# Optimization experiments

Measured on AMD Instinct MI355X. Metric: run time of the kernel, lower is better.

The kernel has to match this reference:

```python
import jax, jax.numpy as jnp
import numpy as np

B, S, C = 4, 4096, 1024   # batch, input_size (seq len), channels
H, D, DK = 16, 64, 256    # nhead, head dim, dim_k (Linformer projection)


def setup_inputs() -> dict:
    key = jax.random.key(0)
    ks = jax.random.split(key, 9)
    s_in = 1.0 / np.sqrt(C)
    s_e = 1.0 / np.sqrt(S)
    return {
        'x':   jax.random.normal(ks[0], (B, S, C), jnp.float32),
        # per-head Q/K/V projection weights (Linear(channels, dim, bias=False))
        'Wq':  jax.random.normal(ks[1], (H, D, C), jnp.float32) * s_in,
        'Wk':  jax.random.normal(ks[2], (H, D, C), jnp.float32) * s_in,
        'Wv':  jax.random.normal(ks[3], (H, D, C), jnp.float32) * s_in,
        # shared (layerwise) E/F Linear(input_size, dim_k) with bias
        'E_w': jax.random.normal(ks[4], (DK, S), jnp.float32) * s_e,
        'E_b': jnp.zeros((DK,), jnp.float32),
        'F_w': jax.random.normal(ks[5], (DK, S), jnp.float32) * s_e,
        'F_b': jnp.zeros((DK,), jnp.float32),
        # output projection Linear(dim*nhead, channels)
        'Wo':  jax.random.normal(ks[6], (C, H * D), jnp.float32) * (1.0 / np.sqrt(H * D)),
        'bo':  jnp.zeros((C,), jnp.float32),
    }


def reference(x, Wq, Wk, Wv, E_w, E_b, F_w, F_b, Wo, bo):
    b, s, c = x.shape
    h, d, _ = Wq.shape
    # per-head projections (vectorized over the Python head loop)
    Q = jnp.einsum('bsc,hdc->bhsd', x, Wq)            # [B,H,S,D]
    Kt = jnp.einsum('bsc,hdc->bhds', x, Wk)           # K already transposed: [B,H,D,S]
    Vt = jnp.einsum('bsc,hdc->bhds', x, Wv)           # [B,H,D,S]
    # Linformer low-rank projections along the sequence axis
    Kp = jnp.einsum('bhds,ks->bhdk', Kt, E_w) + E_b   # [B,H,D,DK]
    Vp = jnp.einsum('bhds,ks->bhdk', Vt, F_w) + F_b   # [B,H,D,DK]
    scores = jnp.einsum('bhsd,bhdk->bhsk', Q, Kp) / jnp.sqrt(jnp.asarray(d, x.dtype))
    P = jax.nn.softmax(scores, axis=-1)               # softmax over projected dim_k
    head_out = jnp.einsum('bhsk,bhdk->bhsd', P, Vp)   # [B,H,S,D]
    out = head_out.transpose(0, 2, 1, 3).reshape(b, s, h * d)  # concat heads
    return out @ Wo.T + bo
```

## Files before the change

### kernel.cpp

```cpp
#include <hip/hip_runtime.h>
#include <stdint.h>

typedef __attribute__((ext_vector_type(8))) short bf16x8;
typedef __attribute__((ext_vector_type(4))) float f32x4;
typedef __attribute__((ext_vector_type(16))) float f32x16;

__device__ __forceinline__ unsigned short f2b(float f) {
  union { float f; uint32_t u; } v; v.f = f;
  uint32_t u = v.u;
  return (unsigned short)((u + 0x7FFFu + ((u >> 16) & 1u)) >> 16);
}

__device__ __forceinline__ void gll16(const unsigned short* gsrc, unsigned short* lds_uniform) {
  __builtin_amdgcn_global_load_lds(
      (const __attribute__((address_space(1))) uint32_t*)gsrc,
      (__attribute__((address_space(3))) uint32_t*)lds_uniform,
      16, 0, 0);
}

#define MFMA(a, b, c) __builtin_amdgcn_mfma_f32_16x16x32_bf16((a), (b), (c), 0, 0, 0)
#define MFMA32(a, b, c) __builtin_amdgcn_mfma_f32_32x32x16_bf16((a), (b), (c), 0, 0, 0)

__global__ void cast_x_dual(const float* __restrict__ x,
                            unsigned short* __restrict__ xb,
                            unsigned short* __restrict__ xT) {
  __shared__ unsigned short tile[64][65];
  const int st = blockIdx.x * 64;
  const int ct = blockIdx.y * 64;
  const int b = blockIdx.z;
  const int t = threadIdx.x;
#pragma unroll
  for (int it = 0; it < 4; ++it) {
    int linear = (it * 256 + t) * 4;
    int r = linear >> 6, c = linear & 63;
    float4 v = *(const float4*)(x + ((size_t)(b * 4096 + st + r)) * 1024 + ct + c);
    ushort4 o;
    o.x = f2b(v.x); o.y = f2b(v.y); o.z = f2b(v.z); o.w = f2b(v.w);
    *(ushort4*)(xb + ((size_t)(b * 4096 + st + r)) * 1024 + ct + c) = o;
    tile[r][c] = o.x; tile[r][c + 1] = o.y; tile[r][c + 2] = o.z; tile[r][c + 3] = o.w;
  }
  __syncthreads();
#pragma unroll
  for (int it = 0; it < 4; ++it) {
    int linear = (it * 256 + t) * 4;
    int r = linear >> 6, c = linear & 63;
    ushort4 o;
    o.x = tile[c][r]; o.y = tile[c + 1][r]; o.z = tile[c + 2][r]; o.w = tile[c + 3][r];
    *(ushort4*)(xT + ((size_t)b * 1024 + ct + r) * 4096 + st + c) = o;
  }
}

__global__ void cast6(const float* __restrict__ s0, const float* __restrict__ s1,
                      const float* __restrict__ s2, const float* __restrict__ s3,
                      const float* __restrict__ s4, const float* __restrict__ s5,
                      const float* __restrict__ E_b, const float* __restrict__ F_b,
                      unsigned short* __restrict__ d0, unsigned short* __restrict__ d1,
                      unsigned short* __restrict__ d2, unsigned short* __restrict__ d3,
                      unsigned short* __restrict__ d4, unsigned short* __restrict__ d5,
                      float* __restrict__ EFbias) {
  if (blockIdx.y == 6) {
    if (blockIdx.x == 0) {
      int t = threadIdx.x;
      EFbias[t] = E_b[t];
      EFbias[256 + t] = F_b[t];
    }
    return;
  }
  const float* src; unsigned short* dst; float sc = 1.0f;
  switch (blockIdx.y) {
    case 0: src = s0; dst = d0; sc = 0.18033688011112042f; break;
    case 1: src = s1; dst = d1; break;
    case 2: src = s2; dst = d2; break;
    case 3: src = s3; dst = d3; break;
    case 4: src = s4; dst = d4; break;
    default: src = s5; dst = d5; break;
  }
  int i = (blockIdx.x * 256 + threadIdx.x) * 4;
  float4 v = *(const float4*)(src + i);
  ushort4 o;
  o.x = f2b(v.x * sc); o.y = f2b(v.y * sc); o.z = f2b(v.z * sc); o.w = f2b(v.w * sc);
  *(ushort4*)(dst + i) = o;
}

template <int BIAS, bool OBF16>
__global__ __launch_bounds__(512, 1) void gemm_bt256(
    const unsigned short* __restrict__ A, const unsigned short* __restrict__ B,
    void* __restrict__ Cout, const float* __restrict__ bias,
    int K, int lda, int ldb, int ldc) {
  __shared__ unsigned short Asm_[4][256 * 32];
  __shared__ unsigned short Bsm_[4][256 * 32];
  const int tid = threadIdx.x;
  const int wave = tid >> 6, lane = tid & 63;
  const int g = (lane >> 4) & 3, l15 = lane & 15;
  const int wmi = wave >> 2, wni = wave & 3;
  const int bm = blockIdx.x * 256, bn = blockIdx.y * 256;

  const int c0 = wave * 2;
  const int rr0 = c0 * 16 + (lane >> 2);
  const int rr1 = rr0 + 16;
  const int sl0 = (lane & 3) ^ ((rr0 >> 1) & 3);
  const int sl1 = (lane & 3) ^ ((rr1 >> 1) & 3);

#define STG(T, BUF)                                                                   \
  {                                                                                   \
    int kt_ = (T) * 32;                                                               \
    gll16(A + (size_t)(bm + rr0) * lda + kt_ + sl0 * 8, Asm_[BUF] + c0 * 512);        \
    gll16(B + (size_t)(bn + rr0) * ldb + kt_ + sl0 * 8, Bsm_[BUF] + c0 * 512);        \
    gll16(A + (size_t)(bm + rr1) * lda + kt_ + sl1 * 8, Asm_[BUF] + (c0 + 1) * 512);  \
    gll16(B + (size_t)(bn + rr1) * ldb + kt_ + sl1 * 8, Bsm_[BUF] + (c0 + 1) * 512);  \
  }

  f32x4 acc[8][4];
#pragma unroll
  for (int i = 0; i < 8; ++i)
#pragma unroll
    for (int j = 0; j < 4; ++j) acc[i][j] = (f32x4){0.f, 0.f, 0.f, 0.f};

  const int nt = K >> 5;
  STG(0, 0);
  if (nt > 1) STG(1, 1);
  if (nt > 2) STG(2, 2);
  asm volatile("s_waitcnt vmcnt(8)" ::: "memory");
  __builtin_amdgcn_s_barrier();
  asm volatile("" ::: "memory");

  for (int t = 0; t < nt; ++t) {
    const int cur = t & 3;
    const char* Ac = (const char*)Asm_[cur];
    const char* Bc = (const char*)Bsm_[cur];

    bf16x8 afr[8], bfr[4];
#pragma unroll
    for (int mf = 0; mf < 8; ++mf) {
      int m = wmi * 128 + mf * 16 + l15;
      afr[mf] = *(const bf16x8*)(Ac + m * 64 + ((g ^ ((m >> 1) & 3)) << 4));
    }
#pragma unroll
    for (int nf = 0; nf < 4; ++nf) {
      int n = wni * 64 + nf * 16 + l15;
      bfr[nf] = *(const bf16x8*)(Bc + n * 64 + ((g ^ ((n >> 1) & 3)) << 4));
    }

    if (t + 3 < nt) STG(t + 3, (t + 3) & 3);

    __builtin_amdgcn_s_setprio(1);
#pragma unroll
    for (int mf = 0; mf < 8; ++mf)
#pragma unroll
      for (int nf = 0; nf < 4; ++nf)
        acc[mf][nf] = MFMA(afr[mf], bfr[nf], acc[mf][nf]);
    __builtin_amdgcn_s_setprio(0);

    if (t + 3 < nt)      asm volatile("s_waitcnt vmcnt(8)" ::: "memory");
    else if (t + 2 < nt) asm volatile("s_waitcnt vmcnt(4)" ::: "memory");
    else                 asm volatile("s_waitcnt vmcnt(0)" ::: "memory");
    __builtin_amdgcn_s_barrier();
    asm volatile("" ::: "memory");
  }
#undef STG

#pragma unroll
  for (int mf = 0; mf < 8; ++mf)
#pragma unroll
    for (int r = 0; r < 4; ++r) {
      int row = bm + wmi * 128 + mf * 16 + g * 4 + r;
      float rb = (BIAS == 1) ? bias[row] : 0.f;
#pragma unroll
      for (int nf = 0; nf < 4; ++nf) {
        int col = bn + wni * 64 + nf * 16 + l15;
        float v = acc[mf][nf][r] + rb + ((BIAS == 2) ? bias[col] : 0.f);
        if (OBF16) ((unsigned short*)Cout)[(size_t)row * ldc + col] = f2b(v);
        else       ((float*)Cout)[(size_t)row * ldc + col] = v;
      }
    }
}

__global__ __launch_bounds__(256, 2) void gemm_xef_splitk(
    const unsigned short* __restrict__ A,
    const unsigned short* __restrict__ B,
    float* __restrict__ Cpart) {
  __shared__ unsigned short Asm_[2][128 * 32];
  __shared__ unsigned short Bsm_[2][128 * 32];
  const int tid = threadIdx.x;
  const int wave = tid >> 6, lane = tid & 63;
  const int g = lane >> 4, l15 = lane & 15;
  const int bm = blockIdx.x * 128, bn = blockIdx.y * 128;
  const int z = blockIdx.z, split = z >> 2, b = z & 3;
  const unsigned short* Ab = A + split * 1024;
  const unsigned short* Bb = B + (size_t)b * 1024 * 4096 + split * 1024;
  const int wm = (wave >> 1) * 64, wn = (wave & 1) * 64;

  const int rr0 = wave * 16 + (lane >> 2);
  const int rr1 = rr0 + 64;
  const int sl0 = (lane & 3) ^ ((rr0 >> 1) & 3);
  const int sl1 = (lane & 3) ^ ((rr1 >> 1) & 3);

#define XEF_STAGE(T, BUF)                                                           \
  {                                                                                 \
    int kt_ = (T) * 32;                                                             \
    gll16(Ab + (size_t)(bm + rr0) * 4096 + kt_ + sl0 * 8, Asm_[BUF] + wave * 512);  \
    gll16(Bb + (size_t)(bn + rr0) * 4096 + kt_ + sl0 * 8, Bsm_[BUF] + wave * 512);  \
    gll16(Ab + (size_t)(bm + rr1) * 4096 + kt_ + sl1 * 8, Asm_[BUF] + (wave + 4) * 512); \
    gll16(Bb + (size_t)(bn + rr1) * 4096 + kt_ + sl1 * 8, Bsm_[BUF] + (wave + 4) * 512); \
  }

  f32x4 acc[4][4];
#pragma unroll
  for (int i = 0; i < 4; ++i)
#pragma unroll
    for (int j = 0; j < 4; ++j) acc[i][j] = (f32x4){0.f, 0.f, 0.f, 0.f};

  const int nt = 32;
  XEF_STAGE(0, 0);
  for (int t = 0; t < nt; ++t) {
    const int cur = t & 1;
    if (t + 1 < nt) {
      XEF_STAGE(t + 1, cur ^ 1);
      asm volatile("s_waitcnt vmcnt(4)" ::: "memory");
    } else {
      asm volatile("s_waitcnt vmcnt(0)" ::: "memory");
    }
    __builtin_amdgcn_s_barrier();
    asm volatile("" ::: "memory");

    bf16x8 af[4], bfr[4];
    const char* Ac = (const char*)Asm_[cur];
    const char* Bc = (const char*)Bsm_[cur];
#pragma unroll
    for (int mi = 0; mi < 4; ++mi) {
      int m = wm + mi * 16 + l15;
      af[mi] = *(const bf16x8*)(Ac + m * 64 + ((g ^ ((m >> 1) & 3)) << 4));
    }
#pragma unroll
    for (int ni = 0; ni < 4; ++ni) {
      int n = wn + ni * 16 + l15;
      bfr[ni] = *(const bf16x8*)(Bc + n * 64 + ((g ^ ((n >> 1) & 3)) << 4));
    }
#pragma unroll
    for (int mi = 0; mi < 4; ++mi)
#pragma unroll
      for (int ni = 0; ni < 4; ++ni)
        acc[mi][ni] = MFMA(af[mi], bfr[ni], acc[mi][ni]);

    asm volatile("" ::: "memory");
    __builtin_amdgcn_s_barrier();
  }
#undef XEF_STAGE

  float* C = Cpart + (size_t)z * (512 * 1024);
#pragma unroll
  for (int mi = 0; mi < 4; ++mi)
#pragma unroll
    for (int r = 0; r < 4; ++r) {
      int row = bm + wm + mi * 16 + g * 4 + r;
#pragma unroll
      for (int ni = 0; ni < 4; ++ni) {
        int col = bn + wn + ni * 16 + l15;
        C[(size_t)row * 1024 + col] = acc[mi][ni][r];
      }
    }
}

__global__ void reduce_xef(const float* __restrict__ P,
                           const float* __restrict__ bias,
                           unsigned short* __restrict__ out) {
  int t = blockIdx.x * 256 + threadIdx.x;
  size_t flat = (size_t)t * 4;
  float4 s = *(const float4*)(P + flat);
#pragma unroll
  for (int sp = 1; sp < 4; ++sp) {
    float4 v = *(const float4*)(P + (size_t)sp * 2097152 + flat);
    s.x += v.x; s.y += v.y; s.z += v.z; s.w += v.w;
  }
  float rb = bias[(flat >> 10) & 511];
  ushort4 o;
  o.x = f2b(s.x + rb); o.y = f2b(s.y + rb);
  o.z = f2b(s.z + rb); o.w = f2b(s.w + rb);
  *(ushort4*)(out + flat) = o;
}

template <int BIAS, bool OBF16, int CMODE>
__global__ __launch_bounds__(256, 4) void gemm_bt64(
    const unsigned short* __restrict__ A, const unsigned short* __restrict__ B,
    void* __restrict__ Cout, const float* __restrict__ bias,
    int M, int N, int K, int lda, int ldb, int ldc,
    long long sA, long long sB, long long sC) {
  __shared__ unsigned short Asm_[2][64 * 32];
  __shared__ unsigned short Bsm_[2][64 * 32];
  const int tid = threadIdx.x;
  const int wave = tid >> 6, lane = tid & 63;
  const int g = lane >> 4, l15 = lane & 15;
  const int bm = blockIdx.x * 64, bn = blockIdx.y * 64;
  const unsigned short* Ab = A + (size_t)blockIdx.z * sA;
  const unsigned short* Bb = B + (size_t)blockIdx.z * sB;
  const int wm = (wave >> 1) * 32, wn = (wave & 1) * 32;

  const int rr = wave * 16 + (lane >> 2);
  const int sl = (lane & 3) ^ ((rr >> 1) & 3);

#define BT64_STAGE(T, BUF)                                                      \
  {                                                                             \
    int kt_ = (T) * 32;                                                         \
    gll16(Ab + (size_t)(bm + rr) * lda + kt_ + sl * 8, Asm_[BUF] + wave * 512); \
    gll16(Bb + (size_t)(bn + rr) * ldb + kt_ + sl * 8, Bsm_[BUF] + wave * 512); \
  }

  f32x4 acc[2][2];
#pragma unroll
  for (int i = 0; i < 2; ++i)
#pragma unroll
    for (int j = 0; j < 2; ++j) acc[i][j] = (f32x4){0.f, 0.f, 0.f, 0.f};

  const int nt = K >> 5;
  BT64_STAGE(0, 0);
  for (int t = 0; t < nt; ++t) {
    const int cur = t & 1;
    if (t + 1 < nt) {
      BT64_STAGE(t + 1, cur ^ 1);
      asm volatile("s_waitcnt vmcnt(2)" ::: "memory");
    } else {
      asm volatile("s_waitcnt vmcnt(0)" ::: "memory");
    }
    __builtin_amdgcn_s_barrier();
    asm volatile("" ::: "memory");

    bf16x8 af[2], bfr[2];
    const char* Ac = (const char*)Asm_[cur];
    const char* Bc = (const char*)Bsm_[cur];
#pragma unroll
    for (int mi = 0; mi < 2; ++mi) {
      int m = wm + mi * 16 + l15;
      af[mi] = *(const bf16x8*)(Ac + m * 64 + ((g ^ ((m >> 1) & 3)) << 4));
    }
#pragma unroll
    for (int ni = 0; ni < 2; ++ni) {
      int n = wn + ni * 16 + l15;
      bfr[ni] = *(const bf16x8*)(Bc + n * 64 + ((g ^ ((n >> 1) & 3)) << 4));
    }
#pragma unroll
    for (int mi = 0; mi < 2; ++mi)
#pragma unroll
      for (int ni = 0; ni < 2; ++ni)
        acc[mi][ni] = MFMA(af[mi], bfr[ni], acc[mi][ni]);

    asm volatile("" ::: "memory");
    __builtin_amdgcn_s_barrier();
  }
#undef BT64_STAGE

#pragma unroll
  for (int mi = 0; mi < 2; ++mi)
#pragma unroll
    for (int r = 0; r < 4; ++r) {
      int row = bm + wm + mi * 16 + g * 4 + r;
      float rb = (BIAS == 1) ? bias[row] : 0.f;
#pragma unroll
      for (int ni = 0; ni < 2; ++ni) {
        int col = bn + wn + ni * 16 + l15;
        float v = acc[mi][ni][r] + rb + ((BIAS == 2) ? bias[col] : 0.f);
        size_t idx;
        if (CMODE == 1) {
          idx = (size_t)(col >> 6) * ((size_t)M * 64) + (size_t)row * 64 + (col & 63);
        } else if (CMODE == 2) {
          int cl = col & 15;
          int cp = (cl & 3) | ((cl & 4) << 1) | ((cl & 8) >> 1);
          idx = (size_t)row * ldc + (col & ~15) + cp;
        } else {
          idx = (size_t)row * ldc + col;
        }
        if (OBF16) ((unsigned short*)Cout + (size_t)blockIdx.z * sC)[idx] = f2b(v);
        else       ((float*)Cout + (size_t)blockIdx.z * sC)[idx] = v;
      }
    }
}

__global__ __launch_bounds__(512, 4) void attn_kernel(
    const unsigned short* __restrict__ q,
    const unsigned short* __restrict__ kp,
    const unsigned short* __restrict__ vp,
    unsigned short* __restrict__ ho) {
  __shared__ unsigned short Ksm[256 * 64];
  __shared__ float Lsm[8 * 32];

  const int tid = threadIdx.x;
  const int wave = tid >> 6, lane = tid & 63;
  const int l31 = lane & 31, hi = lane >> 5;
  const int x = blockIdx.x;
  const int bh = (x & 7) + ((x >> 7) << 3);
  const int qq = (x >> 3) & 15;
  const int b = bh >> 4, h = bh & 15;
  const int s0 = qq * 256;

  const unsigned short* kph = kp + (size_t)bh * (256 * 64);
  const unsigned short* vph = vp + (size_t)bh * (64 * 256);

  {
    const int r = (lane >> 3), sl = (lane & 7) ^ (lane >> 3);
#pragma unroll
    for (int it = 0; it < 4; ++it) {
      int c = it * 8 + wave;
      gll16(kph + (c * 8 + r) * 64 + sl * 8, Ksm + c * 512);
    }
  }

  const int srow = s0 + wave * 32 + l31;
  const unsigned short* qrow = q + (size_t)(b * 4096 + srow) * 1024 + h * 64;
  bf16x8 qf[4];
#pragma unroll
  for (int dc = 0; dc < 4; ++dc)
    qf[dc] = *(const bf16x8*)(qrow + dc * 16 + hi * 8);

  __syncthreads();

  f32x16 ho0 = {0,0,0,0,0,0,0,0,0,0,0,0,0,0,0,0};
  f32x16 ho1 = {0,0,0,0,0,0,0,0,0,0,0,0,0,0,0,0};
  float sum = 0.f;

#pragma unroll
  for (int t = 0; t < 8; ++t) {
    bf16x8 vf00 = *(const bf16x8*)(vph + (size_t)l31 * 256 + (t * 2 + 0) * 16 + hi * 8);
    bf16x8 vf01 = *(const bf16x8*)(vph + (size_t)l31 * 256 + (t * 2 + 1) * 16 + hi * 8);
    bf16x8 vf10 = *(const bf16x8*)(vph + (size_t)(32 + l31) * 256 + (t * 2 + 0) * 16 + hi * 8);
    bf16x8 vf11 = *(const bf16x8*)(vph + (size_t)(32 + l31) * 256 + (t * 2 + 1) * 16 + hi * 8);

    f32x16 qk = {0,0,0,0,0,0,0,0,0,0,0,0,0,0,0,0};
    const int krow = t * 32 + l31;
    const char* kbase = (const char*)Ksm + krow * 128;
#pragma unroll
    for (int dc = 0; dc < 4; ++dc) {
      bf16x8 kf = *(const bf16x8*)(kbase + (((dc * 2 + hi) ^ (l31 & 7)) << 4));
      qk = MFMA32(kf, qf[dc], qk);
    }

    uint32_t pk[8];
#pragma unroll
    for (int j = 0; j < 8; ++j) {
      float e0 = exp2f(qk[2 * j]);
      float e1 = exp2f(qk[2 * j + 1]);
      sum += e0 + e1;
      asm("v_cvt_pk_bf16_f32 %0, %1, %2" : "=v"(pk[j]) : "v"(e0), "v"(e1));
    }
    union { uint32_t u[4]; bf16x8 v; } ua, ub;
    ua.u[0] = pk[0]; ua.u[1] = pk[1]; ua.u[2] = pk[2]; ua.u[3] = pk[3];
    ub.u[0] = pk[4]; ub.u[1] = pk[5]; ub.u[2] = pk[6]; ub.u[7 - 7] = ub.u[0];
    ub.u[0] = pk[4]; ub.u[1] = pk[5]; ub.u[2] = pk[6]; ub.u[3] = pk[7];

    ho0 = MFMA32(ua.v, vf00, ho0);
    ho0 = MFMA32(ub.v, vf01, ho0);
    ho1 = MFMA32(ua.v, vf10, ho1);
    ho1 = MFMA32(ub.v, vf11, ho1);
  }

  sum += __shfl_xor(sum, 32);
  if (lane < 32) Lsm[wave * 32 + lane] = sum;

  float rl[16];
#pragma unroll
  for (int g = 0; g < 4; ++g) {
    float4 d4 = *(const float4*)&Lsm[wave * 32 + g * 8 + hi * 4];
    rl[g * 4 + 0] = __builtin_amdgcn_rcpf(d4.x);
    rl[g * 4 + 1] = __builtin_amdgcn_rcpf(d4.y);
    rl[g * 4 + 2] = __builtin_amdgcn_rcpf(d4.z);
    rl[g * 4 + 3] = __builtin_amdgcn_rcpf(d4.w);
  }

  unsigned short* hob = ho + (size_t)(b * 4096 + s0 + wave * 32) * 1024 + h * 64 + l31;
#pragma unroll
  for (int reg = 0; reg < 16; ++reg) {
    int srw = (reg & 3) + 8 * (reg >> 2) + 4 * hi;
    hob[(size_t)srw * 1024]      = f2b(ho0[reg] * rl[reg]);
    hob[(size_t)srw * 1024 + 32] = f2b(ho1[reg] * rl[reg]);
  }
}

extern "C" void kernel_launch(void* const* d_in, const int* in_sizes, int n_in,
                              void* d_out, int out_size, void* d_ws, size_t ws_size,
                              hipStream_t stream) {
  (void)in_sizes; (void)n_in; (void)out_size; (void)ws_size;
  const float* x   = (const float*)d_in[0];
  const float* Wq  = (const float*)d_in[1];
  const float* Wk  = (const float*)d_in[2];
  const float* Wv  = (const float*)d_in[3];
  const float* E_w = (const float*)d_in[4];
  const float* E_b = (const float*)d_in[5];
  const float* F_w = (const float*)d_in[6];
  const float* F_b = (const float*)d_in[7];
  const float* Wo  = (const float*)d_in[8];
  const float* bo  = (const float*)d_in[9];
  float* out = (float*)d_out;

  char* ws = (char*)d_ws;
  unsigned short* xb   = (unsigned short*)(ws);
  unsigned short* xT   = (unsigned short*)(ws + 33554432);
  unsigned short* Qb   = (unsigned short*)(ws + 67108864);
  unsigned short* Wqb  = (unsigned short*)(ws + 100663296);
  unsigned short* Wkb  = (unsigned short*)(ws + 102760448);
  unsigned short* Wvb  = (unsigned short*)(ws + 104857600);
  unsigned short* Wob  = (unsigned short*)(ws + 106954752);
  unsigned short* EFb  = (unsigned short*)(ws + 109051904);
  unsigned short* xEF  = (unsigned short*)(ws + 113246208);
  unsigned short* Kp   = (unsigned short*)(ws + 117440512);
  unsigned short* Vp   = (unsigned short*)(ws + 119537664);
  float*          EFbias = (float*)(ws + 121634816);
  float*          Ppart  = (float*)(ws + 121700352);
  unsigned short* HO   = xb;

  cast_x_dual<<<dim3(64, 16, 4), 256, 0, stream>>>(x, xb, xT);
  cast6<<<dim3(1024, 7), 256, 0, stream>>>(
      Wq, Wk, Wv, E_w, F_w, Wo, E_b, F_b,
      Wqb, Wkb, Wvb, EFb, EFb + 2097152 / 2, Wob, EFbias);

  gemm_bt256<0, true><<<dim3(64, 4), 512, 0, stream>>>(
      xb, Wqb, Qb, nullptr, 1024, 1024, 1024, 1024);

  gemm_xef_splitk<<<dim3(4, 8, 16), 256, 0, stream>>>(EFb, xT, Ppart);
  reduce_xef<<<dim3(2048, 1, 1), 256, 0, stream>>>(Ppart, EFbias, xEF);

  gemm_bt64<0, true, 1><<<dim3(4, 16, 4), 256, 0, stream>>>(
      xEF, Wkb, Kp, nullptr, 256, 1024, 1024, 1024, 1024, 1024,
      512LL * 1024, 0LL, 256LL * 1024);

  gemm_bt64<0, true, 2><<<dim3(16, 4, 4), 256, 0, stream>>>(
      Wvb, xEF + 256 * 1024, Vp, nullptr, 1024, 256, 1024, 1024, 1024, 256,
      0LL, 512LL * 1024, 1024LL * 256);

  attn_kernel<<<dim3(1024, 1, 1), 512, 0, stream>>>(Qb, Kp, Vp, HO);

  gemm_bt256<2, false><<<dim3(64, 4), 512, 0, stream>>>(
      HO, Wob, out, bo, 1024, 1024, 1024, 1024);
}
```

Before: 216.7 us.

## Shrink GEMM tiles to 128x256 with 3-stage pipeline; compute softmax sums via MFMA

The Q and output-projection GEMMs move from a 256x256 tile with a 4-stage LDS pipeline to a 128x256 tile with 3 stages. This doubles the grid to 512 blocks and allows two blocks per CU, which should improve occupancy and load balance across the 256 CUs. In the attention kernel, softmax row sums are now taken with an extra MFMA against a ones vector, replacing the scalar sums, cross-lane shuffle and LDS exchange. The trade-off is less operand reuse per GEMM tile and extra MFMA work in attention. The row sums are also now taken over the bf16-rounded probabilities rather than the fp32 values.

```diff
diff --git a/kernel.cpp b/kernel.cpp
--- a/kernel.cpp
+++ b/kernel.cpp
@@ -83,56 +83,55 @@
 }
 
 template <int BIAS, bool OBF16>
-__global__ __launch_bounds__(512, 1) void gemm_bt256(
+__global__ __launch_bounds__(512, 2) void gemm_bt128(
     const unsigned short* __restrict__ A, const unsigned short* __restrict__ B,
     void* __restrict__ Cout, const float* __restrict__ bias,
     int K, int lda, int ldb, int ldc) {
-  __shared__ unsigned short Asm_[4][256 * 32];
-  __shared__ unsigned short Bsm_[4][256 * 32];
+  __shared__ unsigned short Asm_[3][128 * 32];
+  __shared__ unsigned short Bsm_[3][256 * 32];
   const int tid = threadIdx.x;
   const int wave = tid >> 6, lane = tid & 63;
   const int g = (lane >> 4) & 3, l15 = lane & 15;
   const int wmi = wave >> 2, wni = wave & 3;
-  const int bm = blockIdx.x * 256, bn = blockIdx.y * 256;
-
-  const int c0 = wave * 2;
-  const int rr0 = c0 * 16 + (lane >> 2);
-  const int rr1 = rr0 + 16;
-  const int sl0 = (lane & 3) ^ ((rr0 >> 1) & 3);
-  const int sl1 = (lane & 3) ^ ((rr1 >> 1) & 3);
-
-#define STG(T, BUF)                                                                   \
-  {                                                                                   \
-    int kt_ = (T) * 32;                                                               \
-    gll16(A + (size_t)(bm + rr0) * lda + kt_ + sl0 * 8, Asm_[BUF] + c0 * 512);        \
-    gll16(B + (size_t)(bn + rr0) * ldb + kt_ + sl0 * 8, Bsm_[BUF] + c0 * 512);        \
-    gll16(A + (size_t)(bm + rr1) * lda + kt_ + sl1 * 8, Asm_[BUF] + (c0 + 1) * 512);  \
-    gll16(B + (size_t)(bn + rr1) * ldb + kt_ + sl1 * 8, Bsm_[BUF] + (c0 + 1) * 512);  \
-  }
-
-  f32x4 acc[8][4];
-#pragma unroll
-  for (int i = 0; i < 8; ++i)
+  const int bm = blockIdx.x * 128, bn = blockIdx.y * 256;
+
+  const int rrA  = wave * 16 + (lane >> 2);
+  const int slA  = (lane & 3) ^ ((rrA >> 1) & 3);
+  const int rrB0 = (wave * 2) * 16 + (lane >> 2);
+  const int rrB1 = rrB0 + 16;
+  const int slB0 = (lane & 3) ^ ((rrB0 >> 1) & 3);
+  const int slB1 = (lane & 3) ^ ((rrB1 >> 1) & 3);
+
+#define STG(T, BUF)                                                                     \
+  {                                                                                     \
+    int kt_ = (T) * 32;                                                                 \
+    gll16(A + (size_t)(bm + rrA) * lda + kt_ + slA * 8, Asm_[BUF] + wave * 512);        \
+    gll16(B + (size_t)(bn + rrB0) * ldb + kt_ + slB0 * 8, Bsm_[BUF] + (wave * 2) * 512);\
+    gll16(B + (size_t)(bn + rrB1) * ldb + kt_ + slB1 * 8, Bsm_[BUF] + (wave * 2 + 1) * 512);\
+  }
+
+  f32x4 acc[4][4];
+#pragma unroll
+  for (int i = 0; i < 4; ++i)
 #pragma unroll
     for (int j = 0; j < 4; ++j) acc[i][j] = (f32x4){0.f, 0.f, 0.f, 0.f};
 
   const int nt = K >> 5;
   STG(0, 0);
   if (nt > 1) STG(1, 1);
-  if (nt > 2) STG(2, 2);
-  asm volatile("s_waitcnt vmcnt(8)" ::: "memory");
+  asm volatile("s_waitcnt vmcnt(3)" ::: "memory");
   __builtin_amdgcn_s_barrier();
   asm volatile("" ::: "memory");
 
   for (int t = 0; t < nt; ++t) {
-    const int cur = t & 3;
+    const int cur = t % 3;
     const char* Ac = (const char*)Asm_[cur];
     const char* Bc = (const char*)Bsm_[cur];
 
-    bf16x8 afr[8], bfr[4];
-#pragma unroll
-    for (int mf = 0; mf < 8; ++mf) {
-      int m = wmi * 128 + mf * 16 + l15;
+    bf16x8 afr[4], bfr[4];
+#pragma unroll
+    for (int mf = 0; mf < 4; ++mf) {
+      int m = wmi * 64 + mf * 16 + l15;
       afr[mf] = *(const bf16x8*)(Ac + m * 64 + ((g ^ ((m >> 1) & 3)) << 4));
     }
 #pragma unroll
@@ -141,29 +140,28 @@
       bfr[nf] = *(const bf16x8*)(Bc + n * 64 + ((g ^ ((n >> 1) & 3)) << 4));
     }
 
-    if (t + 3 < nt) STG(t + 3, (t + 3) & 3);
+    if (t + 2 < nt) STG(t + 2, (t + 2) % 3);
 
     __builtin_amdgcn_s_setprio(1);
 #pragma unroll
-    for (int mf = 0; mf < 8; ++mf)
+    for (int mf = 0; mf < 4; ++mf)
 #pragma unroll
       for (int nf = 0; nf < 4; ++nf)
         acc[mf][nf] = MFMA(afr[mf], bfr[nf], acc[mf][nf]);
     __builtin_amdgcn_s_setprio(0);
 
-    if (t + 3 < nt)      asm volatile("s_waitcnt vmcnt(8)" ::: "memory");
-    else if (t + 2 < nt) asm volatile("s_waitcnt vmcnt(4)" ::: "memory");
-    else                 asm volatile("s_waitcnt vmcnt(0)" ::: "memory");
+    if (t + 2 < nt) asm volatile("s_waitcnt vmcnt(3)" ::: "memory");
+    else            asm volatile("s_waitcnt vmcnt(0)" ::: "memory");
     __builtin_amdgcn_s_barrier();
     asm volatile("" ::: "memory");
   }
 #undef STG
 
 #pragma unroll
-  for (int mf = 0; mf < 8; ++mf)
+  for (int mf = 0; mf < 4; ++mf)
 #pragma unroll
     for (int r = 0; r < 4; ++r) {
-      int row = bm + wmi * 128 + mf * 16 + g * 4 + r;
+      int row = bm + wmi * 64 + mf * 16 + g * 4 + r;
       float rb = (BIAS == 1) ? bias[row] : 0.f;
 #pragma unroll
       for (int nf = 0; nf < 4; ++nf) {
@@ -380,7 +378,6 @@
     const unsigned short* __restrict__ vp,
     unsigned short* __restrict__ ho) {
   __shared__ unsigned short Ksm[256 * 64];
-  __shared__ float Lsm[8 * 32];
 
   const int tid = threadIdx.x;
   const int wave = tid >> 6, lane = tid & 63;
@@ -410,11 +407,15 @@
   for (int dc = 0; dc < 4; ++dc)
     qf[dc] = *(const bf16x8*)(qrow + dc * 16 + hi * 8);
 
+  bf16x8 ones;
+#pragma unroll
+  for (int j = 0; j < 8; ++j) ones[j] = (short)0x3F80;
+
   __syncthreads();
 
   f32x16 ho0 = {0,0,0,0,0,0,0,0,0,0,0,0,0,0,0,0};
   f32x16 ho1 = {0,0,0,0,0,0,0,0,0,0,0,0,0,0,0,0};
-  float sum = 0.f;
+  f32x16 sumacc = {0,0,0,0,0,0,0,0,0,0,0,0,0,0,0,0};
 
 #pragma unroll
   for (int t = 0; t < 8; ++t) {
@@ -437,32 +438,24 @@
     for (int j = 0; j < 8; ++j) {
       float e0 = exp2f(qk[2 * j]);
       float e1 = exp2f(qk[2 * j + 1]);
-      sum += e0 + e1;
       asm("v_cvt_pk_bf16_f32 %0, %1, %2" : "=v"(pk[j]) : "v"(e0), "v"(e1));
     }
     union { uint32_t u[4]; bf16x8 v; } ua, ub;
     ua.u[0] = pk[0]; ua.u[1] = pk[1]; ua.u[2] = pk[2]; ua.u[3] = pk[3];
-    ub.u[0] = pk[4]; ub.u[1] = pk[5]; ub.u[2] = pk[6]; ub.u[7 - 7] = ub.u[0];
     ub.u[0] = pk[4]; ub.u[1] = pk[5]; ub.u[2] = pk[6]; ub.u[3] = pk[7];
 
     ho0 = MFMA32(ua.v, vf00, ho0);
     ho0 = MFMA32(ub.v, vf01, ho0);
     ho1 = MFMA32(ua.v, vf10, ho1);
     ho1 = MFMA32(ub.v, vf11, ho1);
-  }
-
-  sum += __shfl_xor(sum, 32);
-  if (lane < 32) Lsm[wave * 32 + lane] = sum;
+    sumacc = MFMA32(ua.v, ones, sumacc);
+    sumacc = MFMA32(ub.v, ones, sumacc);
+  }
 
   float rl[16];
 #pragma unroll
-  for (int g = 0; g < 4; ++g) {
-    float4 d4 = *(const float4*)&Lsm[wave * 32 + g * 8 + hi * 4];
-    rl[g * 4 + 0] = __builtin_amdgcn_rcpf(d4.x);
-    rl[g * 4 + 1] = __builtin_amdgcn_rcpf(d4.y);
-    rl[g * 4 + 2] = __builtin_amdgcn_rcpf(d4.z);
-    rl[g * 4 + 3] = __builtin_amdgcn_rcpf(d4.w);
-  }
+  for (int reg = 0; reg < 16; ++reg)
+    rl[reg] = __builtin_amdgcn_rcpf(sumacc[reg]);
 
   unsigned short* hob = ho + (size_t)(b * 4096 + s0 + wave * 32) * 1024 + h * 64 + l31;
 #pragma unroll
@@ -510,7 +503,7 @@
       Wq, Wk, Wv, E_w, F_w, Wo, E_b, F_b,
       Wqb, Wkb, Wvb, EFb, EFb + 2097152 / 2, Wob, EFbias);
 
-  gemm_bt256<0, true><<<dim3(64, 4), 512, 0, stream>>>(
+  gemm_bt128<0, true><<<dim3(128, 4), 512, 0, stream>>>(
       xb, Wqb, Qb, nullptr, 1024, 1024, 1024, 1024);
 
   gemm_xef_splitk<<<dim3(4, 8, 16), 256, 0, stream>>>(EFb, xT, Ppart);
@@ -526,6 +519,6 @@
 
   attn_kernel<<<dim3(1024, 1, 1), 512, 0, stream>>>(Qb, Kp, Vp, HO);
 
-  gemm_bt256<2, false><<<dim3(64, 4), 512, 0, stream>>>(
+  gemm_bt128<2, false><<<dim3(128, 4), 512, 0, stream>>>(
       HO, Wob, out, bo, 1024, 1024, 1024, 1024);
 }
```

Result: slower. 222.3 us (+2.6%).

## Stage V tile in LDS and compute softmax row sums via MFMA

Applied to the files above, without the earlier changes.

The attention kernel now loads the per-head projected V tile into swizzled shared memory with async global-to-LDS loads, instead of having every wave read V fragments straight from global memory. The softmax denominators are computed by an extra MFMA against a ones vector, which replaces the scalar accumulation, the cross-lane shuffle and the LDS round trip for the sums. Launch bounds drop from 4 to 2 blocks per SM because LDS use doubles. This lowers occupancy and adds two MFMAs per iteration, and the sums now come from bf16-rounded exponentials.

```diff
diff --git a/kernel.cpp b/kernel.cpp
--- a/kernel.cpp
+++ b/kernel.cpp
@@ -374,13 +374,13 @@
     }
 }
 
-__global__ __launch_bounds__(512, 4) void attn_kernel(
+__global__ __launch_bounds__(512, 2) void attn_kernel(
     const unsigned short* __restrict__ q,
     const unsigned short* __restrict__ kp,
     const unsigned short* __restrict__ vp,
     unsigned short* __restrict__ ho) {
   __shared__ unsigned short Ksm[256 * 64];
-  __shared__ float Lsm[8 * 32];
+  __shared__ unsigned short Vsm[64 * 256];
 
   const int tid = threadIdx.x;
   const int wave = tid >> 6, lane = tid & 63;
@@ -402,6 +402,16 @@
       gll16(kph + (c * 8 + r) * 64 + sl * 8, Ksm + c * 512);
     }
   }
+  {
+    const int rv = lane >> 5;
+#pragma unroll
+    for (int it = 0; it < 4; ++it) {
+      int c = it * 8 + wave;
+      int row = c * 2 + rv;
+      int sl = (lane & 31) ^ (row & 7);
+      gll16(vph + (size_t)row * 256 + sl * 8, Vsm + c * 512);
+    }
+  }
 
   const int srow = s0 + wave * 32 + l31;
   const unsigned short* qrow = q + (size_t)(b * 4096 + srow) * 1024 + h * 64;
@@ -410,18 +420,23 @@
   for (int dc = 0; dc < 4; ++dc)
     qf[dc] = *(const bf16x8*)(qrow + dc * 16 + hi * 8);
 
+  bf16x8 ones;
+#pragma unroll
+  for (int j = 0; j < 8; ++j) ones[j] = (short)0x3F80;
+
   __syncthreads();
 
   f32x16 ho0 = {0,0,0,0,0,0,0,0,0,0,0,0,0,0,0,0};
   f32x16 ho1 = {0,0,0,0,0,0,0,0,0,0,0,0,0,0,0,0};
-  float sum = 0.f;
-
+  f32x16 sumacc = {0,0,0,0,0,0,0,0,0,0,0,0,0,0,0,0};
+
+  const int vsw0 = l31 & 7;
 #pragma unroll
   for (int t = 0; t < 8; ++t) {
-    bf16x8 vf00 = *(const bf16x8*)(vph + (size_t)l31 * 256 + (t * 2 + 0) * 16 + hi * 8);
-    bf16x8 vf01 = *(const bf16x8*)(vph + (size_t)l31 * 256 + (t * 2 + 1) * 16 + hi * 8);
-    bf16x8 vf10 = *(const bf16x8*)(vph + (size_t)(32 + l31) * 256 + (t * 2 + 0) * 16 + hi * 8);
-    bf16x8 vf11 = *(const bf16x8*)(vph + (size_t)(32 + l31) * 256 + (t * 2 + 1) * 16 + hi * 8);
+    bf16x8 vf00 = *(const bf16x8*)((const char*)Vsm + l31 * 512 + (((t * 4 + hi) ^ vsw0) << 4));
+    bf16x8 vf01 = *(const bf16x8*)((const char*)Vsm + l31 * 512 + (((t * 4 + 2 + hi) ^ vsw0) << 4));
+    bf16x8 vf10 = *(const bf16x8*)((const char*)Vsm + (32 + l31) * 512 + (((t * 4 + hi) ^ vsw0) << 4));
+    bf16x8 vf11 = *(const bf16x8*)((const char*)Vsm + (32 + l31) * 512 + (((t * 4 + 2 + hi) ^ vsw0) << 4));
 
     f32x16 qk = {0,0,0,0,0,0,0,0,0,0,0,0,0,0,0,0};
     const int krow = t * 32 + l31;
@@ -437,32 +452,24 @@
     for (int j = 0; j < 8; ++j) {
       float e0 = exp2f(qk[2 * j]);
       float e1 = exp2f(qk[2 * j + 1]);
-      sum += e0 + e1;
       asm("v_cvt_pk_bf16_f32 %0, %1, %2" : "=v"(pk[j]) : "v"(e0), "v"(e1));
     }
     union { uint32_t u[4]; bf16x8 v; } ua, ub;
     ua.u[0] = pk[0]; ua.u[1] = pk[1]; ua.u[2] = pk[2]; ua.u[3] = pk[3];
-    ub.u[0] = pk[4]; ub.u[1] = pk[5]; ub.u[2] = pk[6]; ub.u[7 - 7] = ub.u[0];
     ub.u[0] = pk[4]; ub.u[1] = pk[5]; ub.u[2] = pk[6]; ub.u[3] = pk[7];
 
     ho0 = MFMA32(ua.v, vf00, ho0);
     ho0 = MFMA32(ub.v, vf01, ho0);
     ho1 = MFMA32(ua.v, vf10, ho1);
     ho1 = MFMA32(ub.v, vf11, ho1);
-  }
-
-  sum += __shfl_xor(sum, 32);
-  if (lane < 32) Lsm[wave * 32 + lane] = sum;
+    sumacc = MFMA32(ua.v, ones, sumacc);
+    sumacc = MFMA32(ub.v, ones, sumacc);
+  }
 
   float rl[16];
 #pragma unroll
-  for (int g = 0; g < 4; ++g) {
-    float4 d4 = *(const float4*)&Lsm[wave * 32 + g * 8 + hi * 4];
-    rl[g * 4 + 0] = __builtin_amdgcn_rcpf(d4.x);
-    rl[g * 4 + 1] = __builtin_amdgcn_rcpf(d4.y);
-    rl[g * 4 + 2] = __builtin_amdgcn_rcpf(d4.z);
-    rl[g * 4 + 3] = __builtin_amdgcn_rcpf(d4.w);
-  }
+  for (int reg = 0; reg < 16; ++reg)
+    rl[reg] = __builtin_amdgcn_rcpf(sumacc[reg]);
 
   unsigned short* hob = ho + (size_t)(b * 4096 + s0 + wave * 32) * 1024 + h * 64 + l31;
 #pragma unroll
```

Result: faster. 206.5 us (-4.7%).
